# Kernel optimization log

Measured on AMD Instinct MI355X. Metric: run time of the kernel, lower is better.

Reference implementation:

```python
import jax, jax.numpy as jnp
import numpy as np

B, T, N, F, UNITS = 64, 12, 512, 64, 64

def setup_inputs() -> dict:
    key = jax.random.key(0)
    ks = jax.random.split(key, 9)
    inputs = jax.random.normal(ks[0], (B, T, N, F), dtype=jnp.float32)
    # binary k-hop adjacency mask with self loops (K.to_dense(calculate_adjacency_k(...)))
    A = (jax.random.uniform(ks[1], (N, N)) < 0.05).astype(jnp.float32)
    A = jnp.maximum(A, jnp.eye(N, dtype=jnp.float32))
    W1 = jax.random.normal(ks[2], (T, 1), dtype=jnp.float32) * 0.3
    W2 = jax.random.normal(ks[3], (F, T), dtype=jnp.float32) * 0.1
    W3 = jax.random.normal(ks[4], (F, 1), dtype=jnp.float32) * 0.1
    Ve = jax.random.normal(ks[5], (N, N), dtype=jnp.float32) * 0.05
    be = jax.random.normal(ks[6], (N, N), dtype=jnp.float32) * 0.05
    kernel = jax.random.normal(ks[7], (F, UNITS), dtype=jnp.float32) * 0.1
    bias = jax.random.normal(ks[8], (UNITS,), dtype=jnp.float32) * 0.1
    return {"inputs": inputs, "A": A, "W1": W1, "W2": W2, "W3": W3,
            "Ve": Ve, "be": be, "kernel": kernel, "bias": bias}

def reference(inputs, A, W1, W2, W3, Ve, be, kernel, bias):
    # inputs: (B, T, N, F)
    # lhs: permute->(B,N,F,T), dot W1, squeeze, dot W2 -> (B, N, T)
    r1 = jnp.einsum('btnf,t->bnf', inputs, W1[:, 0])
    lhs = jnp.einsum('bnf,ft->bnt', r1, W2)
    # rhs: dot W3, squeeze -> (B, T, N)
    rhs = jnp.einsum('btnf,f->btn', inputs, W3[:, 0])
    # batch_dot -> (B, N, N)
    product = jnp.einsum('bnt,btm->bnm', lhs, rhs)
    E = jnp.einsum('jk,bkm->bjm', Ve, jax.nn.sigmoid(product + be))
    masked = E + (-1e16) * (1.0 - A)            # adjacency mask
    attn = jax.nn.softmax(masked, axis=-1)       # (B, N, N)
    # graph conv: (B,N,N) x (B,T,N,F) -> (B,T,N,F)
    conv = jnp.einsum('bjk,btkf->btjf', attn, inputs)
    out = jnp.einsum('btjf,fu->btju', conv, kernel) + bias
    return out  # activation=None -> linear
```

## Files before the change

### kernel.cpp

```cpp
#include <hip/hip_runtime.h>
#include <hip/hip_bf16.h>
#include <cstdint>

constexpr int BB = 64;
constexpr int TT = 12;
constexpr int NN = 512;
constexpr int FF = 64;
constexpr int UU = 64;
constexpr int MAXNZ = 128;

constexpr size_t OF_LHS   = 0;
constexpr size_t OF_RHS   = 393216;
constexpr size_t OF_BET   = 786432;
constexpr size_t OF_EVALS = 1048576;
constexpr size_t OB_NNZ   = 20971520;
constexpr size_t OB_CIDX  = 20973568;
constexpr size_t OB_CCNT  = 21235712;
constexpr size_t OB_COLJ  = 21237760;
constexpr size_t OB_XT    = 21516288;
constexpr size_t XT_BYTES = (size_t)BB * NN * TT * FF * 2;
constexpr size_t OB_KF    = 71847936;
constexpr size_t KF_BYTES = 8 * 64 * 8 * 2;

typedef __attribute__((ext_vector_type(8))) short bf16x8;
typedef __attribute__((ext_vector_type(4))) float f32x4;

__device__ __forceinline__ float wred_sum(float v) {
  #pragma unroll
  for (int off = 32; off; off >>= 1) v += __shfl_xor(v, off, 64);
  return v;
}

__device__ __forceinline__ float bflo(unsigned u) {
  return __uint_as_float(u << 16);
}
__device__ __forceinline__ float bfhi(unsigned u) {
  return __uint_as_float(u & 0xFFFF0000u);
}

__global__ __launch_bounds__(256) void k_lhs_rhs(
    const float* __restrict__ x, const float* __restrict__ W1,
    const float* __restrict__ W2, const float* __restrict__ W3,
    float* __restrict__ lhs, float* __restrict__ rhsS,
    unsigned short* __restrict__ xT)
{
  int unit = blockIdx.x * 4 + (threadIdx.x >> 6);
  int lane = threadIdx.x & 63;
  int b = unit >> 9, n = unit & 511;

  const float* xb = x + ((size_t)b * TT * NN + n) * FF + lane;
  float xv[12];
  #pragma unroll
  for (int t = 0; t < 12; ++t) xv[t] = xb[(size_t)t * NN * FF];

  if (xT) {
    unsigned short* xo = xT + (size_t)unit * (TT * FF) + lane;
    #pragma unroll
    for (int t = 0; t < 12; ++t) {
      __hip_bfloat16 h = __float2bfloat16(xv[t]);
      xo[t * FF] = *reinterpret_cast<unsigned short*>(&h);
    }
  }

  float r1 = 0.f;
  #pragma unroll
  for (int t = 0; t < 12; ++t) r1 += xv[t] * W1[t];

  float w3 = W3[lane];

  float myl = 0.f, myr = 0.f;
  #pragma unroll
  for (int t = 0; t < 12; ++t) {
    float a = r1 * W2[lane * 12 + t];
    float c = xv[t] * w3;
    a = wred_sum(a);
    c = wred_sum(c);
    if (lane == t) { myl = a; myr = c; }
  }
  if (lane < 12) {
    lhs[(size_t)unit * 12 + lane]  = myl;
    rhsS[(size_t)unit * 12 + lane] = myr;
  }
}

__global__ __launch_bounds__(256) void k_transpose(
    const float* __restrict__ be, float* __restrict__ beT,
    const float* __restrict__ K, unsigned short* __restrict__ KF)
{
  if (blockIdx.x == NN * NN / 256) {
    if (KF) {
      for (int idx = threadIdx.x; idx < 512; idx += 256) {
        int frag = idx >> 6, l = idx & 63;
        int kk = frag >> 2, nt = frag & 3;
        int u = nt * 16 + (l & 15);
        unsigned short* dst = KF + (size_t)idx * 8;
        for (int e = 0; e < 8; ++e) {
          int f = kk * 32 + (l >> 4) * 8 + e;
          __hip_bfloat16 h = __float2bfloat16(K[f * 64 + u]);
          dst[e] = *reinterpret_cast<unsigned short*>(&h);
        }
      }
    }
    return;
  }
  int i = blockIdx.x * 256 + threadIdx.x;
  int k = i >> 9, m = i & 511;
  beT[m * 512 + k] = be[i];
}

__global__ void k_build_idx(const float* __restrict__ A,
                            int* __restrict__ nnz, int* __restrict__ cidx)
{
  int j = blockIdx.x;
  int lane = threadIdx.x;
  unsigned long long lt = (1ull << lane) - 1ull;
  int base = 0;
  for (int c = 0; c < 8; ++c) {
    int m = c * 64 + lane;
    bool p = A[(size_t)j * 512 + m] > 0.5f;
    unsigned long long mask = __ballot(p);
    int pos = base + __popcll(mask & lt);
    if (p && pos < MAXNZ) cidx[j * MAXNZ + pos] = m;
    base += __popcll(mask);
  }
  if (lane == 0) nnz[j] = base > MAXNZ ? MAXNZ : base;
}

__global__ void k_build_col(const int* __restrict__ nnz, const int* __restrict__ cidx,
                            int* __restrict__ ccnt, unsigned* __restrict__ colj)
{
  int j = blockIdx.x;
  int lane = threadIdx.x;
  int cnt = nnz[j];
  for (int s = lane; s < cnt; s += 64) {
    int m = cidx[j * MAXNZ + s];
    int pos = atomicAdd(&ccnt[m], 1);
    if (pos < MAXNZ) colj[m * MAXNZ + pos] = (unsigned)j | ((unsigned)s << 16);
  }
}

__global__ __launch_bounds__(256) void k_product_E4(
    const float* __restrict__ lhs, const float* __restrict__ rhsS,
    const float* __restrict__ beT, const float* __restrict__ Ve,
    const int* __restrict__ ccnt, const unsigned* __restrict__ colj,
    float* __restrict__ evals)
{
  int b  = blockIdx.x;
  int mc = blockIdx.y;

  __shared__ __align__(16) float sL[16][512];
  __shared__ float rh[16 * 12];

  int tid = threadIdx.x;

  float l0[12], l1[12];
  {
    const float* p0 = lhs + ((size_t)b * 512 + tid) * 12;
    const float* p1 = lhs + ((size_t)b * 512 + tid + 256) * 12;
    #pragma unroll
    for (int t = 0; t < 12; ++t) { l0[t] = p0[t]; l1[t] = p1[t]; }
  }
  if (tid < 192) rh[tid] = rhsS[((size_t)b * 512 + mc * 16) * 12 + tid];
  __syncthreads();

  #pragma unroll 4
  for (int mm = 0; mm < 16; ++mm) {
    int m = mc * 16 + mm;
    float p0 = beT[m * 512 + tid];
    float p1 = beT[m * 512 + tid + 256];
    const float* rw = &rh[mm * 12];
    #pragma unroll
    for (int t = 0; t < 12; ++t) {
      p0 = fmaf(l0[t], rw[t], p0);
      p1 = fmaf(l1[t], rw[t], p1);
    }
    sL[mm][tid]       = 1.0f / (1.0f + __expf(-p0));
    sL[mm][tid + 256] = 1.0f / (1.0f + __expf(-p1));
  }
  __syncthreads();

  int gi = tid >> 4, lg = tid & 15;
  int m = mc * 16 + gi;
  int cnt = ccnt[m];
  if (cnt > MAXNZ) cnt = MAXNZ;
  const float4* sw4 = (const float4*)sL[gi];

  int e = 0;
  for (; e + 1 < cnt; e += 2) {
    unsigned pk0 = colj[m * MAXNZ + e];
    unsigned pk1 = colj[m * MAXNZ + e + 1];
    int j0 = pk0 & 0xffff, s0 = (int)(pk0 >> 16);
    int j1 = pk1 & 0xffff, s1 = (int)(pk1 >> 16);
    const float4* va = (const float4*)(Ve + (size_t)j0 * 512);
    const float4* vb = (const float4*)(Ve + (size_t)j1 * 512);
    float a = 0.f, c = 0.f;
    #pragma unroll
    for (int i = 0; i < 8; ++i) {
      float4 s4 = sw4[lg + 16 * i];
      float4 v4 = va[lg + 16 * i];
      float4 w4 = vb[lg + 16 * i];
      a = fmaf(v4.x, s4.x, a); a = fmaf(v4.y, s4.y, a);
      a = fmaf(v4.z, s4.z, a); a = fmaf(v4.w, s4.w, a);
      c = fmaf(w4.x, s4.x, c); c = fmaf(w4.y, s4.y, c);
      c = fmaf(w4.z, s4.z, c); c = fmaf(w4.w, s4.w, c);
    }
    #pragma unroll
    for (int off = 8; off; off >>= 1) {
      a += __shfl_xor(a, off, 64);
      c += __shfl_xor(c, off, 64);
    }
    if (lg == 0) {
      evals[((size_t)b * 512 + j0) * MAXNZ + s0] = a;
      evals[((size_t)b * 512 + j1) * MAXNZ + s1] = c;
    }
  }
  if (e < cnt) {
    unsigned pk0 = colj[m * MAXNZ + e];
    int j0 = pk0 & 0xffff, s0 = (int)(pk0 >> 16);
    const float4* va = (const float4*)(Ve + (size_t)j0 * 512);
    float a = 0.f;
    #pragma unroll
    for (int i = 0; i < 8; ++i) {
      float4 s4 = sw4[lg + 16 * i];
      float4 v4 = va[lg + 16 * i];
      a = fmaf(v4.x, s4.x, a); a = fmaf(v4.y, s4.y, a);
      a = fmaf(v4.z, s4.z, a); a = fmaf(v4.w, s4.w, a);
    }
    #pragma unroll
    for (int off = 8; off; off >>= 1) a += __shfl_xor(a, off, 64);
    if (lg == 0) evals[((size_t)b * 512 + j0) * MAXNZ + s0] = a;
  }
}

__global__ __launch_bounds__(256) void k_out12(
    const unsigned short* __restrict__ xT,
    const int* __restrict__ nnz, const int* __restrict__ cidx,
    const float* __restrict__ evals,
    const unsigned short* __restrict__ KF, const float* __restrict__ bias,
    float* __restrict__ out)
{
  int tid = threadIdx.x;
  int wv = tid >> 6, lane = tid & 63;
  int bid = blockIdx.x;
  int sbid = (bid & 7) * 1024 + (bid >> 3);
  int unit = sbid * 4 + wv;
  int b = unit >> 9, j = unit & 511;

  __shared__ unsigned short convB[4][16][80];
  __shared__ float valL[4][MAXNZ];
  __shared__ int   idxL[4][MAXNZ];

  int cnt = nnz[j];
  for (int s = lane; s < cnt; s += 64) {
    idxL[wv][s] = cidx[j * MAXNZ + s];
    valL[wv][s] = evals[(size_t)unit * MAXNZ + s];
  }
  {
    float v0 = lane < cnt        ? valL[wv][lane]      : -__builtin_inff();
    float v1 = (lane + 64) < cnt ? valL[wv][lane + 64] : -__builtin_inff();
    float mx = fmaxf(v0, v1);
    #pragma unroll
    for (int off = 32; off; off >>= 1) mx = fmaxf(mx, __shfl_xor(mx, off, 64));
    float e0 = lane < cnt        ? __expf(v0 - mx) : 0.f;
    float e1 = (lane + 64) < cnt ? __expf(v1 - mx) : 0.f;
    float ssum = wred_sum(e0 + e1);
    float inv = 1.0f / ssum;
    if (lane < cnt)        valL[wv][lane]      = e0 * inv;
    if ((lane + 64) < cnt) valL[wv][lane + 64] = e1 * inv;
  }

  float2 acc[6];
  #pragma unroll
  for (int i = 0; i < 6; ++i) acc[i] = make_float2(0.f, 0.f);

  const unsigned* xb = reinterpret_cast<const unsigned*>(
      xT + (size_t)b * NN * (TT * FF));

  int s = 0;
  for (; s + 1 < cnt; s += 2) {
    int   k0 = idxL[wv][s],     k1 = idxL[wv][s + 1];
    float v0 = valL[wv][s],     v1 = valL[wv][s + 1];
    const unsigned* p0 = xb + k0 * 384 + lane;
    const unsigned* p1 = xb + k1 * 384 + lane;
    unsigned a0 = p0[0],   a1 = p0[64],  a2 = p0[128],
             a3 = p0[192], a4 = p0[256], a5 = p0[320];
    unsigned c0 = p1[0],   c1 = p1[64],  c2 = p1[128],
             c3 = p1[192], c4 = p1[256], c5 = p1[320];
    acc[0].x = fmaf(v0, bflo(a0), acc[0].x); acc[0].y = fmaf(v0, bfhi(a0), acc[0].y);
    acc[1].x = fmaf(v0, bflo(a1), acc[1].x); acc[1].y = fmaf(v0, bfhi(a1), acc[1].y);
    acc[2].x = fmaf(v0, bflo(a2), acc[2].x); acc[2].y = fmaf(v0, bfhi(a2), acc[2].y);
    acc[3].x = fmaf(v0, bflo(a3), acc[3].x); acc[3].y = fmaf(v0, bfhi(a3), acc[3].y);
    acc[4].x = fmaf(v0, bflo(a4), acc[4].x); acc[4].y = fmaf(v0, bfhi(a4), acc[4].y);
    acc[5].x = fmaf(v0, bflo(a5), acc[5].x); acc[5].y = fmaf(v0, bfhi(a5), acc[5].y);
    acc[0].x = fmaf(v1, bflo(c0), acc[0].x); acc[0].y = fmaf(v1, bfhi(c0), acc[0].y);
    acc[1].x = fmaf(v1, bflo(c1), acc[1].x); acc[1].y = fmaf(v1, bfhi(c1), acc[1].y);
    acc[2].x = fmaf(v1, bflo(c2), acc[2].x); acc[2].y = fmaf(v1, bfhi(c2), acc[2].y);
    acc[3].x = fmaf(v1, bflo(c3), acc[3].x); acc[3].y = fmaf(v1, bfhi(c3), acc[3].y);
    acc[4].x = fmaf(v1, bflo(c4), acc[4].x); acc[4].y = fmaf(v1, bfhi(c4), acc[4].y);
    acc[5].x = fmaf(v1, bflo(c5), acc[5].x); acc[5].y = fmaf(v1, bfhi(c5), acc[5].y);
  }
  if (s < cnt) {
    int   k0 = idxL[wv][s];
    float v0 = valL[wv][s];
    const unsigned* p0 = xb + k0 * 384 + lane;
    unsigned a0 = p0[0],   a1 = p0[64],  a2 = p0[128],
             a3 = p0[192], a4 = p0[256], a5 = p0[320];
    acc[0].x = fmaf(v0, bflo(a0), acc[0].x); acc[0].y = fmaf(v0, bfhi(a0), acc[0].y);
    acc[1].x = fmaf(v0, bflo(a1), acc[1].x); acc[1].y = fmaf(v0, bfhi(a1), acc[1].y);
    acc[2].x = fmaf(v0, bflo(a2), acc[2].x); acc[2].y = fmaf(v0, bfhi(a2), acc[2].y);
    acc[3].x = fmaf(v0, bflo(a3), acc[3].x); acc[3].y = fmaf(v0, bfhi(a3), acc[3].y);
    acc[4].x = fmaf(v0, bflo(a4), acc[4].x); acc[4].y = fmaf(v0, bfhi(a4), acc[4].y);
    acc[5].x = fmaf(v0, bflo(a5), acc[5].x); acc[5].y = fmaf(v0, bfhi(a5), acc[5].y);
  }

  int half = lane >> 5, fl = lane & 31;
  {
    unsigned short* cb = &convB[wv][0][0];
    #pragma unroll
    for (int i = 0; i < 6; ++i) {
      int t = 2 * i + half;
      __hip_bfloat16 hx = __float2bfloat16(acc[i].x);
      __hip_bfloat16 hy = __float2bfloat16(acc[i].y);
      unsigned pkd = (unsigned)*reinterpret_cast<unsigned short*>(&hx)
                   | ((unsigned)*reinterpret_cast<unsigned short*>(&hy) << 16);
      *reinterpret_cast<unsigned*>(&cb[t * 80 + fl * 2]) = pkd;
    }
  }

  int arow = lane & 15, agrp = lane >> 4;
  bf16x8 afrag0 = *reinterpret_cast<const bf16x8*>(&convB[wv][arow][agrp * 8]);
  bf16x8 afrag1 = *reinterpret_cast<const bf16x8*>(&convB[wv][arow][32 + agrp * 8]);
  const bf16x8* kf = reinterpret_cast<const bf16x8*>(KF);

  #pragma unroll
  for (int nt = 0; nt < 4; ++nt) {
    f32x4 accT = {0.f, 0.f, 0.f, 0.f};
    accT = __builtin_amdgcn_mfma_f32_16x16x32_bf16(afrag0, kf[(0 * 4 + nt) * 64 + lane], accT, 0, 0, 0);
    accT = __builtin_amdgcn_mfma_f32_16x16x32_bf16(afrag1, kf[(1 * 4 + nt) * 64 + lane], accT, 0, 0, 0);
    int u = nt * 16 + arow;
    float bb = bias[u];
    #pragma unroll
    for (int r = 0; r < 4; ++r) {
      int t = agrp * 4 + r;
      if (t < 12)
        out[((size_t)(b * TT + t) * NN + j) * UU + u] = accT[r] + bb;
    }
  }
}

__global__ __launch_bounds__(256) void k_out3f(
    const float* __restrict__ x,
    const int* __restrict__ nnz, const int* __restrict__ cidx,
    const float* __restrict__ evals,
    const float* __restrict__ K, const float* __restrict__ bias,
    float* __restrict__ out)
{
  int wv = threadIdx.x >> 6, lane = threadIdx.x & 63;
  int bid = blockIdx.x;
  int sbid = (bid & 7) * 1024 + (bid >> 3);
  int unit = sbid * 4 + wv;
  int b = unit >> 9, j = unit & 511;

  __shared__ float convL[4][12][64];
  __shared__ float valL[4][MAXNZ];
  __shared__ int   idxL[4][MAXNZ];

  int cnt = nnz[j];
  for (int s = lane; s < cnt; s += 64) {
    idxL[wv][s] = cidx[j * MAXNZ + s];
    valL[wv][s] = evals[(size_t)unit * MAXNZ + s];
  }
  {
    float v0 = lane < cnt        ? valL[wv][lane]      : -__builtin_inff();
    float v1 = (lane + 64) < cnt ? valL[wv][lane + 64] : -__builtin_inff();
    float mx = fmaxf(v0, v1);
    #pragma unroll
    for (int off = 32; off; off >>= 1) mx = fmaxf(mx, __shfl_xor(mx, off, 64));
    float e0 = lane < cnt        ? __expf(v0 - mx) : 0.f;
    float e1 = (lane + 64) < cnt ? __expf(v1 - mx) : 0.f;
    float ssum = wred_sum(e0 + e1);
    float inv = 1.0f / ssum;
    if (lane < cnt)        valL[wv][lane]      = e0 * inv;
    if ((lane + 64) < cnt) valL[wv][lane + 64] = e1 * inv;
  }

  float acc[12];
  #pragma unroll
  for (int t = 0; t < 12; ++t) acc[t] = 0.f;

  const float* xb = x + (size_t)b * TT * NN * FF + lane;
  for (int s = 0; s < cnt; ++s) {
    float v = valL[wv][s];
    const float* xk = xb + (size_t)idxL[wv][s] * FF;
    #pragma unroll
    for (int t = 0; t < 12; ++t)
      acc[t] = fmaf(v, xk[(size_t)t * NN * FF], acc[t]);
  }
  #pragma unroll
  for (int t = 0; t < 12; ++t) convL[wv][t][lane] = acc[t];

  float bs = bias[lane];
  float o[12];
  #pragma unroll
  for (int t = 0; t < 12; ++t) o[t] = bs;
  __syncthreads();

  #pragma unroll
  for (int ft = 0; ft < 4; ++ft) {
    float kc[16];
    #pragma unroll
    for (int i = 0; i < 16; ++i) kc[i] = K[(ft * 16 + i) * 64 + lane];
    #pragma unroll
    for (int t = 0; t < 12; ++t) {
      const float4* cv = (const float4*)&convL[wv][t][ft * 16];
      float4 c0 = cv[0], c1 = cv[1], c2 = cv[2], c3 = cv[3];
      float o_ = o[t];
      o_ = fmaf(c0.x, kc[0],  o_); o_ = fmaf(c0.y, kc[1],  o_);
      o_ = fmaf(c0.z, kc[2],  o_); o_ = fmaf(c0.w, kc[3],  o_);
      o_ = fmaf(c1.x, kc[4],  o_); o_ = fmaf(c1.y, kc[5],  o_);
      o_ = fmaf(c1.z, kc[6],  o_); o_ = fmaf(c1.w, kc[7],  o_);
      o_ = fmaf(c2.x, kc[8],  o_); o_ = fmaf(c2.y, kc[9],  o_);
      o_ = fmaf(c2.z, kc[10], o_); o_ = fmaf(c2.w, kc[11], o_);
      o_ = fmaf(c3.x, kc[12], o_); o_ = fmaf(c3.y, kc[13], o_);
      o_ = fmaf(c3.z, kc[14], o_); o_ = fmaf(c3.w, kc[15], o_);
      o[t] = o_;
    }
  }

  #pragma unroll
  for (int t = 0; t < 12; ++t)
    out[((size_t)(b * TT + t) * NN + j) * UU + lane] = o[t];
}

extern "C" void kernel_launch(void* const* d_in, const int* in_sizes, int n_in,
                              void* d_out, int out_size, void* d_ws, size_t ws_size,
                              hipStream_t stream)
{
  const float* x    = (const float*)d_in[0];
  const float* A    = (const float*)d_in[1];
  const float* W1   = (const float*)d_in[2];
  const float* W2   = (const float*)d_in[3];
  const float* W3   = (const float*)d_in[4];
  const float* Ve   = (const float*)d_in[5];
  const float* be   = (const float*)d_in[6];
  const float* K    = (const float*)d_in[7];
  const float* bias = (const float*)d_in[8];
  float* out = (float*)d_out;

  char* ws = (char*)d_ws;
  float* lhs   = (float*)ws + OF_LHS;
  float* rhsS  = (float*)ws + OF_RHS;
  float* beT   = (float*)ws + OF_BET;
  float* evals = (float*)ws + OF_EVALS;
  int*      nnz  = (int*)(ws + OB_NNZ);
  int*      cidx = (int*)(ws + OB_CIDX);
  int*      ccnt = (int*)(ws + OB_CCNT);
  unsigned* colj = (unsigned*)(ws + OB_COLJ);
  unsigned short* xT = (unsigned short*)(ws + OB_XT);
  unsigned short* KF = (unsigned short*)(ws + OB_KF);

  const bool use_xt = ws_size >= OB_KF + KF_BYTES;

  hipMemsetAsync(ccnt, 0, NN * sizeof(int), stream);

  k_lhs_rhs<<<dim3(BB * NN / 4), dim3(256), 0, stream>>>(
      x, W1, W2, W3, lhs, rhsS, use_xt ? xT : nullptr);
  k_transpose<<<dim3(NN * NN / 256 + 1), dim3(256), 0, stream>>>(
      be, beT, K, use_xt ? KF : nullptr);
  k_build_idx<<<dim3(NN), dim3(64), 0, stream>>>(A, nnz, cidx);
  k_build_col<<<dim3(NN), dim3(64), 0, stream>>>(nnz, cidx, ccnt, colj);
  k_product_E4<<<dim3(BB, NN / 16), dim3(256), 0, stream>>>(lhs, rhsS, beT, Ve, ccnt, colj, evals);
  if (use_xt)
    k_out12<<<dim3(BB * NN / 4), dim3(256), 0, stream>>>(xT, nnz, cidx, evals, KF, bias, out);
  else
    k_out3f<<<dim3(BB * NN / 4), dim3(256), 0, stream>>>(x, nnz, cidx, evals, K, bias, out);
}
```

Baseline: 222.8 us.

## Halve columns per block and spread each column's nonzeros across a wave

The product/E kernel now handles 8 columns per block instead of 16, which doubles the grid and halves shared memory per block. In the gather phase each wave takes one column at a time, and its four 16-lane groups split that column's nonzero entries between them. Before, a 16-lane group walked one column's whole list alone. This balances uneven per-column nonzero counts inside a wave and raises occupancy, at the cost of recomputing the lhs loads per block and doing more block setup work.

```diff
diff --git a/kernel.cpp b/kernel.cpp
--- a/kernel.cpp
+++ b/kernel.cpp
@@ -139,7 +139,7 @@
   }
 }
 
-__global__ __launch_bounds__(256) void k_product_E4(
+__global__ __launch_bounds__(256) void k_product_E5(
     const float* __restrict__ lhs, const float* __restrict__ rhsS,
     const float* __restrict__ beT, const float* __restrict__ Ve,
     const int* __restrict__ ccnt, const unsigned* __restrict__ colj,
@@ -148,87 +148,91 @@
   int b  = blockIdx.x;
   int mc = blockIdx.y;
 
-  __shared__ __align__(16) float sL[16][512];
-  __shared__ float rh[16 * 12];
+  __shared__ __align__(16) float sL[8][512];
+  __shared__ float rh[8 * 12];
 
   int tid = threadIdx.x;
+  int wave = tid >> 6, lane = tid & 63;
+  int grp = lane >> 4, lg = lane & 15;
 
   float l0[12], l1[12];
   {
     const float* p0 = lhs + ((size_t)b * 512 + tid) * 12;
-    const float* p1 = lhs + ((size_t)b * 512 + tid + 256) * 12;
+    const float* p1 = p0 + 256 * 12;
     #pragma unroll
     for (int t = 0; t < 12; ++t) { l0[t] = p0[t]; l1[t] = p1[t]; }
   }
-  if (tid < 192) rh[tid] = rhsS[((size_t)b * 512 + mc * 16) * 12 + tid];
+  if (tid < 96) rh[tid] = rhsS[((size_t)b * 512 + mc * 8) * 12 + tid];
   __syncthreads();
 
-  #pragma unroll 4
-  for (int mm = 0; mm < 16; ++mm) {
-    int m = mc * 16 + mm;
-    float p0 = beT[m * 512 + tid];
-    float p1 = beT[m * 512 + tid + 256];
+  #pragma unroll
+  for (int mm = 0; mm < 8; ++mm) {
+    int m = mc * 8 + mm;
+    float q0 = beT[m * 512 + tid];
+    float q1 = beT[m * 512 + tid + 256];
     const float* rw = &rh[mm * 12];
     #pragma unroll
     for (int t = 0; t < 12; ++t) {
-      p0 = fmaf(l0[t], rw[t], p0);
-      p1 = fmaf(l1[t], rw[t], p1);
-    }
-    sL[mm][tid]       = 1.0f / (1.0f + __expf(-p0));
-    sL[mm][tid + 256] = 1.0f / (1.0f + __expf(-p1));
+      q0 = fmaf(l0[t], rw[t], q0);
+      q1 = fmaf(l1[t], rw[t], q1);
+    }
+    sL[mm][tid]       = 1.0f / (1.0f + __expf(-q0));
+    sL[mm][tid + 256] = 1.0f / (1.0f + __expf(-q1));
   }
   __syncthreads();
 
-  int gi = tid >> 4, lg = tid & 15;
-  int m = mc * 16 + gi;
-  int cnt = ccnt[m];
-  if (cnt > MAXNZ) cnt = MAXNZ;
-  const float4* sw4 = (const float4*)sL[gi];
-
-  int e = 0;
-  for (; e + 1 < cnt; e += 2) {
-    unsigned pk0 = colj[m * MAXNZ + e];
-    unsigned pk1 = colj[m * MAXNZ + e + 1];
-    int j0 = pk0 & 0xffff, s0 = (int)(pk0 >> 16);
-    int j1 = pk1 & 0xffff, s1 = (int)(pk1 >> 16);
-    const float4* va = (const float4*)(Ve + (size_t)j0 * 512);
-    const float4* vb = (const float4*)(Ve + (size_t)j1 * 512);
-    float a = 0.f, c = 0.f;
-    #pragma unroll
-    for (int i = 0; i < 8; ++i) {
-      float4 s4 = sw4[lg + 16 * i];
-      float4 v4 = va[lg + 16 * i];
-      float4 w4 = vb[lg + 16 * i];
-      a = fmaf(v4.x, s4.x, a); a = fmaf(v4.y, s4.y, a);
-      a = fmaf(v4.z, s4.z, a); a = fmaf(v4.w, s4.w, a);
-      c = fmaf(w4.x, s4.x, c); c = fmaf(w4.y, s4.y, c);
-      c = fmaf(w4.z, s4.z, c); c = fmaf(w4.w, s4.w, c);
-    }
-    #pragma unroll
-    for (int off = 8; off; off >>= 1) {
-      a += __shfl_xor(a, off, 64);
-      c += __shfl_xor(c, off, 64);
-    }
-    if (lg == 0) {
-      evals[((size_t)b * 512 + j0) * MAXNZ + s0] = a;
-      evals[((size_t)b * 512 + j1) * MAXNZ + s1] = c;
-    }
-  }
-  if (e < cnt) {
-    unsigned pk0 = colj[m * MAXNZ + e];
-    int j0 = pk0 & 0xffff, s0 = (int)(pk0 >> 16);
-    const float4* va = (const float4*)(Ve + (size_t)j0 * 512);
-    float a = 0.f;
-    #pragma unroll
-    for (int i = 0; i < 8; ++i) {
-      float4 s4 = sw4[lg + 16 * i];
-      float4 v4 = va[lg + 16 * i];
-      a = fmaf(v4.x, s4.x, a); a = fmaf(v4.y, s4.y, a);
-      a = fmaf(v4.z, s4.z, a); a = fmaf(v4.w, s4.w, a);
-    }
-    #pragma unroll
-    for (int off = 8; off; off >>= 1) a += __shfl_xor(a, off, 64);
-    if (lg == 0) evals[((size_t)b * 512 + j0) * MAXNZ + s0] = a;
+  for (int cc = 0; cc < 2; ++cc) {
+    int mm = wave + cc * 4;
+    int m = mc * 8 + mm;
+    int cnt = ccnt[m];
+    if (cnt > MAXNZ) cnt = MAXNZ;
+    const float4* sw4 = (const float4*)sL[mm];
+    const unsigned* cj = colj + m * MAXNZ;
+
+    int e0 = grp;
+    for (; e0 + 4 < cnt; e0 += 8) {
+      unsigned pk0 = cj[e0], pk1 = cj[e0 + 4];
+      int j0 = pk0 & 0xffff, s0 = (int)(pk0 >> 16);
+      int j1 = pk1 & 0xffff, s1 = (int)(pk1 >> 16);
+      const float4* va = (const float4*)(Ve + (size_t)j0 * 512);
+      const float4* vb = (const float4*)(Ve + (size_t)j1 * 512);
+      float a = 0.f, c = 0.f;
+      #pragma unroll
+      for (int i = 0; i < 8; ++i) {
+        float4 s4 = sw4[lg + 16 * i];
+        float4 v4 = va[lg + 16 * i];
+        float4 w4 = vb[lg + 16 * i];
+        a = fmaf(v4.x, s4.x, a); a = fmaf(v4.y, s4.y, a);
+        a = fmaf(v4.z, s4.z, a); a = fmaf(v4.w, s4.w, a);
+        c = fmaf(w4.x, s4.x, c); c = fmaf(w4.y, s4.y, c);
+        c = fmaf(w4.z, s4.z, c); c = fmaf(w4.w, s4.w, c);
+      }
+      #pragma unroll
+      for (int off = 8; off; off >>= 1) {
+        a += __shfl_xor(a, off, 64);
+        c += __shfl_xor(c, off, 64);
+      }
+      if (lg == 0) {
+        evals[((size_t)b * 512 + j0) * MAXNZ + s0] = a;
+        evals[((size_t)b * 512 + j1) * MAXNZ + s1] = c;
+      }
+    }
+    if (e0 < cnt) {
+      unsigned pk0 = cj[e0];
+      int j0 = pk0 & 0xffff, s0 = (int)(pk0 >> 16);
+      const float4* va = (const float4*)(Ve + (size_t)j0 * 512);
+      float a = 0.f;
+      #pragma unroll
+      for (int i = 0; i < 8; ++i) {
+        float4 s4 = sw4[lg + 16 * i];
+        float4 v4 = va[lg + 16 * i];
+        a = fmaf(v4.x, s4.x, a); a = fmaf(v4.y, s4.y, a);
+        a = fmaf(v4.z, s4.z, a); a = fmaf(v4.w, s4.w, a);
+      }
+      #pragma unroll
+      for (int off = 8; off; off >>= 1) a += __shfl_xor(a, off, 64);
+      if (lg == 0) evals[((size_t)b * 512 + j0) * MAXNZ + s0] = a;
+    }
   }
 }
 
@@ -469,7 +473,7 @@
       be, beT, K, use_xt ? KF : nullptr);
   k_build_idx<<<dim3(NN), dim3(64), 0, stream>>>(A, nnz, cidx);
   k_build_col<<<dim3(NN), dim3(64), 0, stream>>>(nnz, cidx, ccnt, colj);
-  k_product_E4<<<dim3(BB, NN / 16), dim3(256), 0, stream>>>(lhs, rhsS, beT, Ve, ccnt, colj, evals);
+  k_product_E5<<<dim3(BB, NN / 8), dim3(256), 0, stream>>>(lhs, rhsS, beT, Ve, ccnt, colj, evals);
   if (use_xt)
     k_out12<<<dim3(BB * NN / 4), dim3(256), 0, stream>>>(xT, nnz, cidx, evals, KF, bias, out);
   else
```

Measured after the change: 218.5 us. Within noise of the previous version (-1.9%).
